# Kernel optimization log

Hardware: AMD Instinct MI355X
Metric: run time of the kernel (lower is better)

Reference implementation:

```python
import jax, jax.numpy as jnp
import numpy as np

B, C, H, W = 8, 64, 256, 256

def setup_inputs() -> dict:
    key = jax.random.key(0)
    ks = jax.random.split(key, 8)
    s = 1.0 / np.sqrt(C)
    return {
        "x": jax.random.normal(ks[0], (B, C, H, W), jnp.float32),
        "Wq": jax.random.normal(ks[1], (C, C), jnp.float32) * s,
        "Wk_spe": jax.random.normal(ks[2], (C,), jnp.float32) * s,
        "Wv_spe": jax.random.normal(ks[3], (C, C), jnp.float32) * s,
        "Wv_spa": jax.random.normal(ks[4], (C, C), jnp.float32) * s,
        "Wup": jax.random.normal(ks[5], (C, C), jnp.float32) * s,
        "Wout": jax.random.normal(ks[6], (C, C), jnp.float32) * s,
        "Wnorm": jax.random.normal(ks[7], (1, 1, 7, 7), jnp.float32) * (1.0 / 7.0),
    }

def _forward(x, Wq, Wk_spe, Wv_spe, Wv_spa, Wup, Wout, Wnorm):
    b, c, h, w = x.shape
    # 1x1 convs as channel GEMMs
    q = jnp.einsum('oc,bchw->bohw', Wq, x).reshape(b, c, h * w)      # [B,C,HW]
    v_spe = jnp.einsum('oc,bchw->bohw', Wv_spe, x)                   # [B,C,H,W]
    v_spa = jnp.einsum('oc,bchw->bohw', Wv_spa, x)                   # [B,C,H,W]
    k_spe = jnp.einsum('c,bchw->bhw', Wk_spe, x).reshape(b, h * w)   # [B,HW]
    k_spe = jax.nn.softmax(k_spe, axis=-1)                           # softmax over spatial
    # spectral (channel) attention: pool q with spatial weights
    attn_spe = jnp.einsum('bcn,bn->bc', q, k_spe)                    # [B,C]
    attn_spe = jnp.einsum('oc,bc->bo', Wup, attn_spe)                # conv_up 1x1
    a = jax.nn.softmax(attn_spe, axis=1)                             # softmax over channels
    out_spe = v_spe * a[:, :, None, None]
    # spatial attention: channel-pool q with a
    attn_spa = jnp.einsum('bc,bcn->bn', a, q).reshape(b, 1, h, w)    # [B,1,H,W]
    attn_spa = jax.lax.conv_general_dilated(
        attn_spa, Wnorm, window_strides=(1, 1), padding=((3, 3), (3, 3)),
        dimension_numbers=('NCHW', 'OIHW', 'NCHW'))
    attn_spa = jax.nn.sigmoid(attn_spa)
    out_spa = attn_spa * v_spa
    out = jnp.einsum('oc,bchw->bohw', Wout, out_spa + out_spe)
    return out

def reference(x, Wq, Wk_spe, Wv_spe, Wv_spa, Wup, Wout, Wnorm):
    return _forward(x, Wq, Wk_spe, Wv_spe, Wv_spa, Wup, Wout, Wnorm)
```

## Files before the change

kernel.cpp:

```cpp
#include <hip/hip_runtime.h>
#include <cstdint>
#include <cstddef>

#define Bn 8
#define Cn 64
#define HWn 65536

#define WS_Z 0
#define WS_XPOOL 8
#define WS_A 520
#define WS_WA 1032
#define WS_M1 1544
#define WS_M2 5640
#define WS_S 38408


__global__ __launch_bounds__(256) void k1(const float* __restrict__ x, const float* __restrict__ Wk,
                                          float* __restrict__ ws) {
  __shared__ float e_s[512];
  __shared__ float red[4];
  int blk = blockIdx.x;
  int b = blk >> 7;
  int base = (blk & 127) << 9;
  int t = threadIdx.x;
  const float* xb = x + (size_t)b * Cn * HWn;
  int n0 = base + t * 2;

  float kx = 0.f, ky = 0.f;
#pragma unroll 16
  for (int c = 0; c < Cn; ++c) {
    float2 xv = *(const float2*)(xb + (size_t)c * HWn + n0);
    float w = Wk[c];
    kx += w * xv.x; ky += w * xv.y;
  }
  float ex = __expf(kx), ey = __expf(ky);
  e_s[t * 2] = ex; e_s[t * 2 + 1] = ey;
  float part = ex + ey;
#pragma unroll
  for (int off = 32; off; off >>= 1) part += __shfl_down(part, off, 64);
  int lane = t & 63, wid = t >> 6;
  if (lane == 0) red[wid] = part;
  __syncthreads();
  if (t == 0) atomicAdd(&ws[WS_Z + b], red[0] + red[1] + red[2] + red[3]);

#pragma unroll 4
  for (int j = 0; j < 16; ++j) {
    int c = wid * 16 + j;
    const float* xc = xb + (size_t)c * HWn + base;
    float acc = 0.f;
#pragma unroll
    for (int rep = 0; rep < 8; ++rep) {
      int idx = rep * 64 + lane;
      acc += xc[idx] * e_s[idx];
    }
#pragma unroll
    for (int off = 32; off; off >>= 1) acc += __shfl_down(acc, off, 64);
    if (lane == 0) atomicAdd(&ws[WS_XPOOL + b * Cn + c], acc);
  }
}

__global__ void k2a(const float* __restrict__ Wq, const float* __restrict__ Wup, float* __restrict__ ws) {
  int b = blockIdx.x;
  int t = threadIdx.x;
  __shared__ float xp_s[64], t1[64], a_s[64];
  float Zb = ws[WS_Z + b];
  xp_s[t] = ws[WS_XPOOL + b * 64 + t] / Zb;
  __syncthreads();
  float acc = 0.f;
#pragma unroll
  for (int i = 0; i < 64; ++i) acc += Wq[t * 64 + i] * xp_s[i];
  t1[t] = acc;
  __syncthreads();
  float acc2 = 0.f;
#pragma unroll
  for (int i = 0; i < 64; ++i) acc2 += Wup[t * 64 + i] * t1[i];
  float m = acc2;
#pragma unroll
  for (int off = 32; off; off >>= 1) m = fmaxf(m, __shfl_xor(m, off, 64));
  float e = __expf(acc2 - m);
  float ssum = e;
#pragma unroll
  for (int off = 32; off; off >>= 1) ssum += __shfl_xor(ssum, off, 64);
  float av = e / ssum;
  ws[WS_A + b * 64 + t] = av;
  a_s[t] = av;
  __syncthreads();
  float wav = 0.f;
#pragma unroll
  for (int o = 0; o < 64; ++o) wav += a_s[o] * Wq[o * 64 + t];
  ws[WS_WA + b * 64 + t] = wav;
}

__global__ __launch_bounds__(256) void k2b(const float* __restrict__ Wout, const float* __restrict__ Wv_spa,
                                           const float* __restrict__ Wv_spe, float* __restrict__ ws) {
  __shared__ float A[4096], Bm[4096];
  int j = blockIdx.x;
  for (int idx = threadIdx.x; idx < 4096; idx += 256) {
    A[idx] = Wout[idx];
    if (j == 0)
      Bm[idx] = Wv_spa[idx];
    else
      Bm[idx] = ws[WS_A + (j - 1) * 64 + (idx >> 6)] * Wv_spe[idx];
  }
  __syncthreads();
  float* dst = (j == 0) ? (ws + WS_M1) : (ws + WS_M2 + (size_t)(j - 1) * 4096);
  for (int oi = threadIdx.x; oi < 4096; oi += 256) {
    int o = oi >> 6, i = oi & 63;
    float acc = 0.f;
#pragma unroll
    for (int c = 0; c < 64; ++c) acc += A[o * 64 + c] * Bm[c * 64 + i];
    dst[i * 64 + o] = acc;
  }
}

__global__ __launch_bounds__(256) void k3(const float* __restrict__ x, const float* __restrict__ ws,
                                          float* __restrict__ out) {
  int blk = blockIdx.x;
  int b = blk >> 7;
  int base = (blk & 127) << 9;
  int n0 = base + threadIdx.x * 2;
  const float* xb = x + (size_t)b * Cn * HWn;
  const float* wa = ws + WS_WA + b * 64;
  float kx = 0.f, ky = 0.f;
#pragma unroll 16
  for (int c = 0; c < Cn; ++c) {
    float2 xv = *(const float2*)(xb + (size_t)c * HWn + n0);
    float w = wa[c];
    kx += w * xv.x; ky += w * xv.y;
  }
  float2 r = {kx, ky};
  *(float2*)(out + ((size_t)(b * Cn + 2)) * HWn + n0) = r;
}

__global__ __launch_bounds__(256) void kconv(const float* __restrict__ Wn, const float* __restrict__ out,
                                             float* __restrict__ dst_base, size_t dst_stride) {
  __shared__ float t[38 * 38];
  int blk = blockIdx.x;
  int b = blk >> 6, ty = (blk >> 3) & 7, tx = blk & 7;
  const float* src = out + ((size_t)(b * Cn + 2)) * HWn;
  float* dstp = dst_base + (size_t)b * dst_stride;
  for (int idx = threadIdx.x; idx < 38 * 38; idx += 256) {
    int ly = idx / 38, lx = idx - ly * 38;
    int gy = ty * 32 + ly - 3, gx = tx * 32 + lx - 3;
    float v = 0.f;
    if (gy >= 0 && gy < 256 && gx >= 0 && gx < 256) v = src[gy * 256 + gx];
    t[idx] = v;
  }
  __syncthreads();
#pragma unroll
  for (int q = 0; q < 4; ++q) {
    int pix = threadIdx.x + q * 256;
    int r = pix >> 5, col = pix & 31;
    float acc = 0.f;
#pragma unroll
    for (int dy = 0; dy < 7; ++dy)
#pragma unroll
      for (int dx = 0; dx < 7; ++dx)
        acc += t[(r + dy) * 38 + (col + dx)] * Wn[dy * 7 + dx];
    float sg = 1.f / (1.f + __expf(-acc));
    dstp[(ty * 32 + r) * 256 + tx * 32 + col] = sg;
  }
}

__global__ __launch_bounds__(256, 4) void k4f(const float* __restrict__ x, const float* __restrict__ ws,
                                              float* __restrict__ out) {
  int d = blockIdx.x;
  int xcd = d & 7;
  int j = d >> 3;
  int oc = j & 3;
  int pg = j >> 2;
  int p = pg * 8 + xcd;
  int b = p >> 6;
  int tile = p & 63;
  int t = threadIdx.x;
  const float* m1t = ws + WS_M1 + oc * 16;
  const float* m2t = ws + WS_M2 + (size_t)b * 4096 + oc * 16;

  int n0 = (tile << 10) + t * 4;
  const float* xb = x + (size_t)b * Cn * HWn;
  float4 s4 = *(const float4*)(ws + WS_S + (size_t)b * HWn + n0);
  float4 acc[16];
#pragma unroll
  for (int o = 0; o < 16; ++o) acc[o] = make_float4(0.f, 0.f, 0.f, 0.f);

#pragma unroll 4
  for (int i = 0; i < 64; ++i) {
    float4 xv = *(const float4*)(xb + (size_t)i * HWn + n0);
    float4 sx;
    sx.x = s4.x * xv.x; sx.y = s4.y * xv.y; sx.z = s4.z * xv.z; sx.w = s4.w * xv.w;
    const float* w1r = m1t + i * 64;
    const float* w2r = m2t + i * 64;
#pragma unroll
    for (int o = 0; o < 16; ++o) {
      float w1 = w1r[o], w2 = w2r[o];
      acc[o].x += w1 * sx.x + w2 * xv.x;
      acc[o].y += w1 * sx.y + w2 * xv.y;
      acc[o].z += w1 * sx.z + w2 * xv.z;
      acc[o].w += w1 * sx.w + w2 * xv.w;
    }
  }
  float* op = out + ((size_t)(b * Cn + oc * 16)) * HWn + n0;
#pragma unroll
  for (int o = 0; o < 16; ++o)
    *(float4*)(op + (size_t)o * HWn) = acc[o];
}

#define MSTRIDE 68
__global__ __launch_bounds__(256) void k4m(const float* __restrict__ x, const float* __restrict__ ws,
                                           float* out) {
  __shared__ float M1T[64 * MSTRIDE];
  __shared__ float M2T[64 * MSTRIDE];
  int blk = blockIdx.x;
  int b = blk >> 6;
  int base = (blk & 63) << 10;
  int t = threadIdx.x;
  const float* m1g = ws + WS_M1;
  const float* m2g = ws + WS_M2 + (size_t)b * 4096;
  for (int idx = t; idx < 4096; idx += 256) {
    int c = idx >> 6, o = idx & 63;
    M1T[c * MSTRIDE + o] = m1g[idx];
    M2T[c * MSTRIDE + o] = m2g[idx];
  }
  __syncthreads();
  int n0 = base + t * 4;
  const float* xb = x + (size_t)b * Cn * HWn;
  float* op = out + ((size_t)(b * Cn)) * HWn + n0;
  float4 s4 = *(const float4*)op;
#pragma unroll
  for (int oc = 0; oc < 4; ++oc) {
    float4 acc[16];
#pragma unroll
    for (int o = 0; o < 16; ++o) acc[o] = make_float4(0.f, 0.f, 0.f, 0.f);
    for (int i = 0; i < 64; ++i) {
      float4 xv = *(const float4*)(xb + (size_t)i * HWn + n0);
      float4 sx;
      sx.x = s4.x * xv.x; sx.y = s4.y * xv.y; sx.z = s4.z * xv.z; sx.w = s4.w * xv.w;
      const float* m1r = M1T + i * MSTRIDE + oc * 16;
      const float* m2r = M2T + i * MSTRIDE + oc * 16;
#pragma unroll
      for (int o = 0; o < 16; ++o) {
        float m1 = m1r[o], m2 = m2r[o];
        acc[o].x += m1 * sx.x + m2 * xv.x;
        acc[o].y += m1 * sx.y + m2 * xv.y;
        acc[o].z += m1 * sx.z + m2 * xv.z;
        acc[o].w += m1 * sx.w + m2 * xv.w;
      }
    }
#pragma unroll
    for (int o = 0; o < 16; ++o)
      *(float4*)(op + (size_t)(oc * 16 + o) * HWn) = acc[o];
  }
}

extern "C" void kernel_launch(void* const* d_in, const int* in_sizes, int n_in,
                              void* d_out, int out_size, void* d_ws, size_t ws_size,
                              hipStream_t stream) {
  const float* x      = (const float*)d_in[0];
  const float* Wq     = (const float*)d_in[1];
  const float* Wk     = (const float*)d_in[2];
  const float* Wv_spe = (const float*)d_in[3];
  const float* Wv_spa = (const float*)d_in[4];
  const float* Wup    = (const float*)d_in[5];
  const float* Wout   = (const float*)d_in[6];
  const float* Wn     = (const float*)d_in[7];
  float* out = (float*)d_out;
  float* ws  = (float*)d_ws;

  bool fast = ws_size >= (size_t)(WS_S + Bn * HWn) * sizeof(float);

  hipMemsetAsync(ws, 0, 520 * sizeof(float), stream);
  k1<<<1024, 256, 0, stream>>>(x, Wk, ws);
  k2a<<<8, 64, 0, stream>>>(Wq, Wup, ws);
  k2b<<<9, 256, 0, stream>>>(Wout, Wv_spa, Wv_spe, ws);
  k3<<<1024, 256, 0, stream>>>(x, ws, out);
  if (fast) {
    kconv<<<512, 256, 0, stream>>>(Wn, out, ws + WS_S, (size_t)HWn);
    k4f<<<2048, 256, 0, stream>>>(x, ws, out);
  } else {
    kconv<<<512, 256, 0, stream>>>(Wn, out, out, (size_t)Cn * HWn);
    k4m<<<512, 256, 0, stream>>>(x, ws, out);
  }
}
```

Baseline: 446.7 us.

## Widen k1/k3 loads to float4, double-buffer k4f x loads, nontemporal output stores

```diff
diff --git a/kernel.cpp b/kernel.cpp
--- a/kernel.cpp
+++ b/kernel.cpp
@@ -14,28 +14,31 @@
 #define WS_M2 5640
 #define WS_S 38408
 
+typedef float f32x4 __attribute__((ext_vector_type(4)));
+
 
 __global__ __launch_bounds__(256) void k1(const float* __restrict__ x, const float* __restrict__ Wk,
                                           float* __restrict__ ws) {
-  __shared__ float e_s[512];
+  __shared__ float e_s[1024];
   __shared__ float red[4];
   int blk = blockIdx.x;
-  int b = blk >> 7;
-  int base = (blk & 127) << 9;
+  int b = blk >> 6;
+  int base = (blk & 63) << 10;
   int t = threadIdx.x;
   const float* xb = x + (size_t)b * Cn * HWn;
-  int n0 = base + t * 2;
-
-  float kx = 0.f, ky = 0.f;
+  int n0 = base + t * 4;
+
+  float kx = 0.f, ky = 0.f, kz = 0.f, kw = 0.f;
 #pragma unroll 16
   for (int c = 0; c < Cn; ++c) {
-    float2 xv = *(const float2*)(xb + (size_t)c * HWn + n0);
+    float4 xv = *(const float4*)(xb + (size_t)c * HWn + n0);
     float w = Wk[c];
-    kx += w * xv.x; ky += w * xv.y;
-  }
-  float ex = __expf(kx), ey = __expf(ky);
-  e_s[t * 2] = ex; e_s[t * 2 + 1] = ey;
-  float part = ex + ey;
+    kx += w * xv.x; ky += w * xv.y; kz += w * xv.z; kw += w * xv.w;
+  }
+  float4 ev;
+  ev.x = __expf(kx); ev.y = __expf(ky); ev.z = __expf(kz); ev.w = __expf(kw);
+  *(float4*)(e_s + t * 4) = ev;
+  float part = ev.x + ev.y + ev.z + ev.w;
 #pragma unroll
   for (int off = 32; off; off >>= 1) part += __shfl_down(part, off, 64);
   int lane = t & 63, wid = t >> 6;
@@ -49,9 +52,11 @@
     const float* xc = xb + (size_t)c * HWn + base;
     float acc = 0.f;
 #pragma unroll
-    for (int rep = 0; rep < 8; ++rep) {
-      int idx = rep * 64 + lane;
-      acc += xc[idx] * e_s[idx];
+    for (int rep = 0; rep < 4; ++rep) {
+      int idx = rep * 256 + lane * 4;
+      float4 xv = *(const float4*)(xc + idx);
+      float4 evv = *(const float4*)(e_s + idx);
+      acc += xv.x * evv.x + xv.y * evv.y + xv.z * evv.z + xv.w * evv.w;
     }
 #pragma unroll
     for (int off = 32; off; off >>= 1) acc += __shfl_down(acc, off, 64);
@@ -116,20 +121,20 @@
 __global__ __launch_bounds__(256) void k3(const float* __restrict__ x, const float* __restrict__ ws,
                                           float* __restrict__ out) {
   int blk = blockIdx.x;
-  int b = blk >> 7;
-  int base = (blk & 127) << 9;
-  int n0 = base + threadIdx.x * 2;
+  int b = blk >> 6;
+  int base = (blk & 63) << 10;
+  int n0 = base + threadIdx.x * 4;
   const float* xb = x + (size_t)b * Cn * HWn;
   const float* wa = ws + WS_WA + b * 64;
-  float kx = 0.f, ky = 0.f;
+  float kx = 0.f, ky = 0.f, kz = 0.f, kw = 0.f;
 #pragma unroll 16
   for (int c = 0; c < Cn; ++c) {
-    float2 xv = *(const float2*)(xb + (size_t)c * HWn + n0);
+    float4 xv = *(const float4*)(xb + (size_t)c * HWn + n0);
     float w = wa[c];
-    kx += w * xv.x; ky += w * xv.y;
-  }
-  float2 r = {kx, ky};
-  *(float2*)(out + ((size_t)(b * Cn + 2)) * HWn + n0) = r;
+    kx += w * xv.x; ky += w * xv.y; kz += w * xv.z; kw += w * xv.w;
+  }
+  float4 r = {kx, ky, kz, kw};
+  *(float4*)(out + ((size_t)(b * Cn + 2)) * HWn + n0) = r;
 }
 
 __global__ __launch_bounds__(256) void kconv(const float* __restrict__ Wn, const float* __restrict__ out,
@@ -162,7 +167,24 @@
   }
 }
 
-__global__ __launch_bounds__(256, 4) void k4f(const float* __restrict__ x, const float* __restrict__ ws,
+#define K4_STEP(xv, i)                                        \
+  {                                                           \
+    const float* w1r = m1t + (i) * 64;                        \
+    const float* w2r = m2t + (i) * 64;                        \
+    float4 sx;                                                \
+    sx.x = s4.x * (xv).x; sx.y = s4.y * (xv).y;               \
+    sx.z = s4.z * (xv).z; sx.w = s4.w * (xv).w;               \
+    _Pragma("unroll")                                         \
+    for (int o = 0; o < 16; ++o) {                            \
+      float w1 = w1r[o], w2 = w2r[o];                         \
+      acc[o].x += w1 * sx.x + w2 * (xv).x;                    \
+      acc[o].y += w1 * sx.y + w2 * (xv).y;                    \
+      acc[o].z += w1 * sx.z + w2 * (xv).z;                    \
+      acc[o].w += w1 * sx.w + w2 * (xv).w;                    \
+    }                                                         \
+  }
+
+__global__ __launch_bounds__(256, 3) void k4f(const float* __restrict__ x, const float* __restrict__ ws,
                                               float* __restrict__ out) {
   int d = blockIdx.x;
   int xcd = d & 7;
@@ -177,32 +199,34 @@
   const float* m2t = ws + WS_M2 + (size_t)b * 4096 + oc * 16;
 
   int n0 = (tile << 10) + t * 4;
-  const float* xb = x + (size_t)b * Cn * HWn;
+  const float* xp = x + (size_t)b * Cn * HWn + n0;
   float4 s4 = *(const float4*)(ws + WS_S + (size_t)b * HWn + n0);
   float4 acc[16];
 #pragma unroll
   for (int o = 0; o < 16; ++o) acc[o] = make_float4(0.f, 0.f, 0.f, 0.f);
 
-#pragma unroll 4
-  for (int i = 0; i < 64; ++i) {
-    float4 xv = *(const float4*)(xb + (size_t)i * HWn + n0);
-    float4 sx;
-    sx.x = s4.x * xv.x; sx.y = s4.y * xv.y; sx.z = s4.z * xv.z; sx.w = s4.w * xv.w;
-    const float* w1r = m1t + i * 64;
-    const float* w2r = m2t + i * 64;
-#pragma unroll
-    for (int o = 0; o < 16; ++o) {
-      float w1 = w1r[o], w2 = w2r[o];
-      acc[o].x += w1 * sx.x + w2 * xv.x;
-      acc[o].y += w1 * sx.y + w2 * xv.y;
-      acc[o].z += w1 * sx.z + w2 * xv.z;
-      acc[o].w += w1 * sx.w + w2 * xv.w;
-    }
-  }
+  float4 xA[4], xB[4];
+#pragma unroll
+  for (int k = 0; k < 4; ++k) xA[k] = *(const float4*)(xp + (size_t)k * HWn);
+
+#pragma unroll 1
+  for (int g = 0; g < 8; ++g) {
+    int cB = g * 8 + 4;
+#pragma unroll
+    for (int k = 0; k < 4; ++k) xB[k] = *(const float4*)(xp + (size_t)(cB + k) * HWn);
+#pragma unroll
+    for (int k = 0; k < 4; ++k) K4_STEP(xA[k], g * 8 + k);
+    int cA = (g < 7) ? (g * 8 + 8) : 0;
+#pragma unroll
+    for (int k = 0; k < 4; ++k) xA[k] = *(const float4*)(xp + (size_t)(cA + k) * HWn);
+#pragma unroll
+    for (int k = 0; k < 4; ++k) K4_STEP(xB[k], cB + k);
+  }
+
   float* op = out + ((size_t)(b * Cn + oc * 16)) * HWn + n0;
 #pragma unroll
   for (int o = 0; o < 16; ++o)
-    *(float4*)(op + (size_t)o * HWn) = acc[o];
+    __builtin_nontemporal_store(*(const f32x4*)&acc[o], (f32x4*)(op + (size_t)o * HWn));
 }
 
 #define MSTRIDE 68
@@ -268,11 +292,11 @@
 
   bool fast = ws_size >= (size_t)(WS_S + Bn * HWn) * sizeof(float);
 
-  hipMemsetAsync(ws, 0, 520 * sizeof(float), stream);
-  k1<<<1024, 256, 0, stream>>>(x, Wk, ws);
+  (void)hipMemsetAsync(ws, 0, 520 * sizeof(float), stream);
+  k1<<<512, 256, 0, stream>>>(x, Wk, ws);
   k2a<<<8, 64, 0, stream>>>(Wq, Wup, ws);
   k2b<<<9, 256, 0, stream>>>(Wout, Wv_spa, Wv_spe, ws);
-  k3<<<1024, 256, 0, stream>>>(x, ws, out);
+  k3<<<512, 256, 0, stream>>>(x, ws, out);
   if (fast) {
     kconv<<<512, 256, 0, stream>>>(Wn, out, ws + WS_S, (size_t)HWn);
     k4f<<<2048, 256, 0, stream>>>(x, ws, out);
```

After: 830.8 us. 86.0% more time.
